# Optimization experiments

Measured on AMD Instinct MI355X. Metric: run time of the kernel, lower is better.

The kernel has to match this reference:

```python
import jax, jax.numpy as jnp
import numpy as np

CHEB_K = 3
HIDDEN = 64
INPUT_DIM = 2
B, N = 16, 307


def setup_inputs() -> dict:
    key = jax.random.key(0)
    ks = jax.random.split(key, 7)
    in_dim = CHEB_K * (INPUT_DIM + HIDDEN)  # 198
    return {
        "G": jax.random.normal(ks[0], (CHEB_K, N, N), jnp.float32) / np.sqrt(N),
        "xt": jax.random.normal(ks[1], (B, N, INPUT_DIM), jnp.float32),
        "h": jax.random.normal(ks[2], (B, N, HIDDEN), jnp.float32),
        "W_conv_gate": jax.random.normal(ks[3], (B, N, in_dim, 2 * HIDDEN), jnp.float32) * 0.05,
        "b_conv_gate": jax.random.normal(ks[4], (B, N, 2 * HIDDEN), jnp.float32) * 0.05,
        "W_update": jax.random.normal(ks[5], (B, N, in_dim, HIDDEN), jnp.float32) * 0.05,
        "b_update": jax.random.normal(ks[6], (B, N, HIDDEN), jnp.float32) * 0.05,
    }


def _st_meta_gcn(G, x, W, b):
    # G: [K,N,N], x: [B,N,I] -> support per hop, concatenated hop-major on feat axis
    bsz, n, i = x.shape
    sup = jnp.einsum('knm,bmi->bnki', G, x)          # [B,N,K,I]
    sup = sup.reshape(bsz, n, G.shape[0] * i)        # matches torch.cat over hops
    return jnp.einsum('bni,bnih->bnh', sup, W) + b


def reference(G, xt, h, W_conv_gate, b_conv_gate, W_update, b_update):
    combined = jnp.concatenate([xt, h], axis=-1)
    gates = jax.nn.sigmoid(_st_meta_gcn(G, combined, W_conv_gate, b_conv_gate))
    z, r = gates[..., :HIDDEN], gates[..., HIDDEN:]
    candidate = jnp.concatenate([xt, r * h], axis=-1)
    n = jnp.tanh(_st_meta_gcn(G, candidate, W_update, b_update))
    return z * n + (1.0 - z) * h
```

## Files before the change

kernel.cpp:

```cpp
#include <hip/hip_runtime.h>
#include <math.h>

#define NB   16
#define NN   307
#define MPAD 308
#define Q4   77
#define KCH  3
#define IND  66
#define KI   198
#define HID  64
#define HG   128

typedef float f32x4 __attribute__((ext_vector_type(4)));

#define OFF_GP  0
#define SZ_GP   (KCH * NN * MPAD)
#define OFF_X1  (OFF_GP + SZ_GP)
#define SZ_X    (NB * Q4 * IND * 4)
#define OFF_X2  (OFF_X1 + SZ_X)
#define OFF_Z   (OFF_X2 + SZ_X)

__global__ void prep_kernel(const float* __restrict__ G,
                            const float* __restrict__ xt,
                            const float* __restrict__ h,
                            float* __restrict__ G_p,
                            float* __restrict__ x1,
                            float* __restrict__ x2) {
    int idx = blockIdx.x * blockDim.x + threadIdx.x;
    if (idx < SZ_GP) {
        int mp = idx % MPAD;
        int kn = idx / MPAD;
        G_p[idx] = (mp < NN) ? G[kn * NN + mp] : 0.f;
    } else if (idx < SZ_GP + SZ_X) {
        int j = idx - SZ_GP;
        int e = j & 3;
        int t = j >> 2;
        int i = t % IND;
        int q = (t / IND) % Q4;
        int b = t / (IND * Q4);
        int m = q * 4 + e;
        float v = 0.f;
        if (m < NN)
            v = (i < 2) ? xt[(b * NN + m) * 2 + i]
                        : h[(b * NN + m) * HID + (i - 2)];
        x1[j] = v;
    } else if (idx < SZ_GP + 2 * SZ_X) {
        int j = idx - SZ_GP - SZ_X;
        int e = j & 3;
        int t = j >> 2;
        int i = t % IND;
        int q = (t / IND) % Q4;
        int b = t / (IND * Q4);
        int m = q * 4 + e;
        float v = 0.f;
        if (m < NN && i < 2) v = xt[(b * NN + m) * 2 + i];
        x2[j] = v;
    }
}

__global__ __launch_bounds__(128) void gate_fused(const float* __restrict__ G_p,
                                                  const float* __restrict__ xT,
                                                  const float* __restrict__ W,
                                                  const float* __restrict__ bias,
                                                  const float* __restrict__ h,
                                                  float* __restrict__ z_out,
                                                  float* __restrict__ xT2) {
    __shared__ float s[KI];
    __shared__ float red[4][HG];
    const int bn  = blockIdx.x;
    const int b   = bn / NN;
    const int n   = bn % NN;
    const int tid = threadIdx.x;
    if (tid < IND) {
        const f32x4* xp = (const f32x4*)xT + (size_t)b * (Q4 * IND) + tid;
        const f32x4* gp = (const f32x4*)G_p + (size_t)n * Q4;
        f32x4 a0 = {0.f, 0.f, 0.f, 0.f}, a1 = a0, a2 = a0;
        #pragma unroll 7
        for (int q = 0; q < Q4; ++q) {
            f32x4 xv = xp[(size_t)q * IND];
            a0 += xv * gp[q];
            a1 += xv * gp[q + (size_t)NN * Q4];
            a2 += xv * gp[q + (size_t)2 * NN * Q4];
        }
        s[tid]           = a0.x + a0.y + a0.z + a0.w;
        s[IND + tid]     = a1.x + a1.y + a1.z + a1.w;
        s[2 * IND + tid] = a2.x + a2.y + a2.z + a2.w;
    }
    __syncthreads();
    const int r  = tid >> 5;
    const int c4 = (tid & 31) * 4;
    const f32x4* Wp = (const f32x4*)(W + (size_t)bn * KI * HG + c4);
    float4 acc = make_float4(0.f, 0.f, 0.f, 0.f);
    #pragma unroll 8
    for (int i = r; i < KI; i += 4) {
        f32x4 w = __builtin_nontemporal_load(Wp + (size_t)i * (HG / 4));
        float sv = s[i];
        acc.x += sv * w.x; acc.y += sv * w.y;
        acc.z += sv * w.z; acc.w += sv * w.w;
    }
    red[r][c4 + 0] = acc.x; red[r][c4 + 1] = acc.y;
    red[r][c4 + 2] = acc.z; red[r][c4 + 3] = acc.w;
    __syncthreads();
    float a = bias[bn * HG + tid] + red[0][tid] + red[1][tid] + red[2][tid] + red[3][tid];
    float g = 1.0f / (1.0f + expf(-a));
    if (tid < HID) {
        z_out[bn * HID + tid] = g;
    } else {
        int hh = tid - HID;
        int q = n >> 2, e = n & 3;
        xT2[(((size_t)b * Q4 + q) * IND + 2 + hh) * 4 + e] = g * h[bn * HID + hh];
    }
}

__global__ __launch_bounds__(128) void update_fused(const float* __restrict__ G_p,
                                                    const float* __restrict__ xT2,
                                                    const float* __restrict__ W,
                                                    const float* __restrict__ bias,
                                                    const float* __restrict__ z,
                                                    const float* __restrict__ h,
                                                    float* __restrict__ out) {
    __shared__ float s[KI];
    __shared__ float red[8][HID];
    const int bn  = blockIdx.x;
    const int b   = bn / NN;
    const int n   = bn % NN;
    const int tid = threadIdx.x;
    if (tid < IND) {
        const f32x4* xp = (const f32x4*)xT2 + (size_t)b * (Q4 * IND) + tid;
        const f32x4* gp = (const f32x4*)G_p + (size_t)n * Q4;
        f32x4 a0 = {0.f, 0.f, 0.f, 0.f}, a1 = a0, a2 = a0;
        #pragma unroll 7
        for (int q = 0; q < Q4; ++q) {
            f32x4 xv = xp[(size_t)q * IND];
            a0 += xv * gp[q];
            a1 += xv * gp[q + (size_t)NN * Q4];
            a2 += xv * gp[q + (size_t)2 * NN * Q4];
        }
        s[tid]           = a0.x + a0.y + a0.z + a0.w;
        s[IND + tid]     = a1.x + a1.y + a1.z + a1.w;
        s[2 * IND + tid] = a2.x + a2.y + a2.z + a2.w;
    }
    __syncthreads();
    const int r  = tid >> 4;
    const int c4 = (tid & 15) * 4;
    const f32x4* Wp = (const f32x4*)(W + (size_t)bn * KI * HID + c4);
    float4 acc = make_float4(0.f, 0.f, 0.f, 0.f);
    #pragma unroll 8
    for (int i = r; i < KI; i += 8) {
        f32x4 w = __builtin_nontemporal_load(Wp + (size_t)i * (HID / 4));
        float sv = s[i];
        acc.x += sv * w.x; acc.y += sv * w.y;
        acc.z += sv * w.z; acc.w += sv * w.w;
    }
    red[r][c4 + 0] = acc.x; red[r][c4 + 1] = acc.y;
    red[r][c4 + 2] = acc.z; red[r][c4 + 3] = acc.w;
    __syncthreads();
    if (tid < HID) {
        float a = bias[bn * HID + tid];
        #pragma unroll
        for (int rr = 0; rr < 8; ++rr) a += red[rr][tid];
        float nn = tanhf(a);
        float zz = z[bn * HID + tid];
        float hv = h[bn * HID + tid];
        out[bn * HID + tid] = zz * nn + (1.f - zz) * hv;
    }
}

extern "C" void kernel_launch(void* const* d_in, const int* in_sizes, int n_in,
                              void* d_out, int out_size, void* d_ws, size_t ws_size,
                              hipStream_t stream) {
    const float* G  = (const float*)d_in[0];
    const float* xt = (const float*)d_in[1];
    const float* h  = (const float*)d_in[2];
    const float* Wg = (const float*)d_in[3];
    const float* bg = (const float*)d_in[4];
    const float* Wu = (const float*)d_in[5];
    const float* bu = (const float*)d_in[6];
    float* out = (float*)d_out;

    float* ws   = (float*)d_ws;
    float* G_p  = ws + OFF_GP;
    float* x1   = ws + OFF_X1;
    float* x2   = ws + OFF_X2;
    float* z    = ws + OFF_Z;

    const int totPrep = SZ_GP + 2 * SZ_X;
    prep_kernel<<<(totPrep + 255) / 256, 256, 0, stream>>>(G, xt, h, G_p, x1, x2);

    gate_fused<<<NB * NN, 128, 0, stream>>>(G_p, x1, Wg, bg, h, z, x2);

    update_fused<<<NB * NN, 128, 0, stream>>>(G_p, x2, Wu, bu, z, h, out);
}
```

Measured before the change: 164.0 us.

## Prefetch per-node weights during graph aggregation and shrink x2 prep to input channels

Each block now issues its first ten weight-row loads into registers, spread across the graph-support loop, so the streaming of W overlaps the G·x aggregation rather than starting after the barrier. All threads run the aggregation loop (clamped index) so every thread can interleave its prefetches, and only the first 66 threads store results. The prep kernel no longer zero-fills all of x2; it writes only the two xt channels, because the gate kernel overwrites the rest. This costs more registers per thread and redundant aggregation work in idle threads.

```diff
diff --git a/kernel.cpp b/kernel.cpp
--- a/kernel.cpp
+++ b/kernel.cpp
@@ -19,6 +19,7 @@
 #define SZ_X    (NB * Q4 * IND * 4)
 #define OFF_X2  (OFF_X1 + SZ_X)
 #define OFF_Z   (OFF_X2 + SZ_X)
+#define SZ_X2I  (NB * Q4 * 2 * 4)
 
 __global__ void prep_kernel(const float* __restrict__ G,
                             const float* __restrict__ xt,
@@ -44,17 +45,17 @@
             v = (i < 2) ? xt[(b * NN + m) * 2 + i]
                         : h[(b * NN + m) * HID + (i - 2)];
         x1[j] = v;
-    } else if (idx < SZ_GP + 2 * SZ_X) {
+    } else if (idx < SZ_GP + SZ_X + SZ_X2I) {
         int j = idx - SZ_GP - SZ_X;
-        int e = j & 3;
-        int t = j >> 2;
-        int i = t % IND;
-        int q = (t / IND) % Q4;
-        int b = t / (IND * Q4);
-        int m = q * 4 + e;
-        float v = 0.f;
-        if (m < NN && i < 2) v = xt[(b * NN + m) * 2 + i];
-        x2[j] = v;
+        int e  = j & 3;
+        int t  = j >> 2;
+        int i  = t & 1;
+        int t2 = t >> 1;
+        int q  = t2 % Q4;
+        int b  = t2 / Q4;
+        int m  = q * 4 + e;
+        float v = (m < NN) ? xt[(b * NN + m) * 2 + i] : 0.f;
+        x2[(((size_t)b * Q4 + q) * IND + i) * 4 + e] = v;
     }
 }
 
@@ -71,33 +72,51 @@
     const int b   = bn / NN;
     const int n   = bn % NN;
     const int tid = threadIdx.x;
+    const int r   = tid >> 5;
+    const int c4  = (tid & 31) * 4;
+    const f32x4* Wp = (const f32x4*)(W + (size_t)bn * KI * HG + c4);
+    const int ii = (tid < IND) ? tid : 0;
+    const f32x4* xp = (const f32x4*)xT + (size_t)b * (Q4 * IND) + ii;
+    const f32x4* gp = (const f32x4*)G_p + (size_t)n * Q4;
+    f32x4 a0 = {0.f, 0.f, 0.f, 0.f}, a1 = a0, a2 = a0;
+    f32x4 w0, w1, w2, w3, w4, w5, w6, w7, w8, w9;
+    #pragma unroll
+    for (int q = 0; q < Q4; ++q) {
+        if (q == 0)  w0 = __builtin_nontemporal_load(Wp + (size_t)(r +  0) * (HG / 4));
+        if (q == 8)  w1 = __builtin_nontemporal_load(Wp + (size_t)(r +  4) * (HG / 4));
+        if (q == 16) w2 = __builtin_nontemporal_load(Wp + (size_t)(r +  8) * (HG / 4));
+        if (q == 24) w3 = __builtin_nontemporal_load(Wp + (size_t)(r + 12) * (HG / 4));
+        if (q == 32) w4 = __builtin_nontemporal_load(Wp + (size_t)(r + 16) * (HG / 4));
+        if (q == 40) w5 = __builtin_nontemporal_load(Wp + (size_t)(r + 20) * (HG / 4));
+        if (q == 48) w6 = __builtin_nontemporal_load(Wp + (size_t)(r + 24) * (HG / 4));
+        if (q == 56) w7 = __builtin_nontemporal_load(Wp + (size_t)(r + 28) * (HG / 4));
+        if (q == 64) w8 = __builtin_nontemporal_load(Wp + (size_t)(r + 32) * (HG / 4));
+        if (q == 72) w9 = __builtin_nontemporal_load(Wp + (size_t)(r + 36) * (HG / 4));
+        f32x4 xv = xp[(size_t)q * IND];
+        a0 += xv * gp[q];
+        a1 += xv * gp[q + (size_t)NN * Q4];
+        a2 += xv * gp[q + (size_t)2 * NN * Q4];
+    }
     if (tid < IND) {
-        const f32x4* xp = (const f32x4*)xT + (size_t)b * (Q4 * IND) + tid;
-        const f32x4* gp = (const f32x4*)G_p + (size_t)n * Q4;
-        f32x4 a0 = {0.f, 0.f, 0.f, 0.f}, a1 = a0, a2 = a0;
-        #pragma unroll 7
-        for (int q = 0; q < Q4; ++q) {
-            f32x4 xv = xp[(size_t)q * IND];
-            a0 += xv * gp[q];
-            a1 += xv * gp[q + (size_t)NN * Q4];
-            a2 += xv * gp[q + (size_t)2 * NN * Q4];
-        }
         s[tid]           = a0.x + a0.y + a0.z + a0.w;
         s[IND + tid]     = a1.x + a1.y + a1.z + a1.w;
         s[2 * IND + tid] = a2.x + a2.y + a2.z + a2.w;
     }
     __syncthreads();
-    const int r  = tid >> 5;
-    const int c4 = (tid & 31) * 4;
-    const f32x4* Wp = (const f32x4*)(W + (size_t)bn * KI * HG + c4);
     float4 acc = make_float4(0.f, 0.f, 0.f, 0.f);
+#define CONS(wv, I) { float sv = s[(I)]; acc.x += sv * (wv).x; acc.y += sv * (wv).y; \
+                      acc.z += sv * (wv).z; acc.w += sv * (wv).w; }
+    CONS(w0, r)      CONS(w1, r + 4)  CONS(w2, r + 8)  CONS(w3, r + 12)
+    CONS(w4, r + 16) CONS(w5, r + 20) CONS(w6, r + 24) CONS(w7, r + 28)
+    CONS(w8, r + 32) CONS(w9, r + 36)
     #pragma unroll 8
-    for (int i = r; i < KI; i += 4) {
+    for (int i = r + 40; i < KI; i += 4) {
         f32x4 w = __builtin_nontemporal_load(Wp + (size_t)i * (HG / 4));
         float sv = s[i];
         acc.x += sv * w.x; acc.y += sv * w.y;
         acc.z += sv * w.z; acc.w += sv * w.w;
     }
+#undef CONS
     red[r][c4 + 0] = acc.x; red[r][c4 + 1] = acc.y;
     red[r][c4 + 2] = acc.z; red[r][c4 + 3] = acc.w;
     __syncthreads();
@@ -125,33 +144,51 @@
     const int b   = bn / NN;
     const int n   = bn % NN;
     const int tid = threadIdx.x;
+    const int r   = tid >> 4;
+    const int c4  = (tid & 15) * 4;
+    const f32x4* Wp = (const f32x4*)(W + (size_t)bn * KI * HID + c4);
+    const int ii = (tid < IND) ? tid : 0;
+    const f32x4* xp = (const f32x4*)xT2 + (size_t)b * (Q4 * IND) + ii;
+    const f32x4* gp = (const f32x4*)G_p + (size_t)n * Q4;
+    f32x4 a0 = {0.f, 0.f, 0.f, 0.f}, a1 = a0, a2 = a0;
+    f32x4 w0, w1, w2, w3, w4, w5, w6, w7, w8, w9;
+    #pragma unroll
+    for (int q = 0; q < Q4; ++q) {
+        if (q == 0)  w0 = __builtin_nontemporal_load(Wp + (size_t)(r +  0) * (HID / 4));
+        if (q == 8)  w1 = __builtin_nontemporal_load(Wp + (size_t)(r +  8) * (HID / 4));
+        if (q == 16) w2 = __builtin_nontemporal_load(Wp + (size_t)(r + 16) * (HID / 4));
+        if (q == 24) w3 = __builtin_nontemporal_load(Wp + (size_t)(r + 24) * (HID / 4));
+        if (q == 32) w4 = __builtin_nontemporal_load(Wp + (size_t)(r + 32) * (HID / 4));
+        if (q == 40) w5 = __builtin_nontemporal_load(Wp + (size_t)(r + 40) * (HID / 4));
+        if (q == 48) w6 = __builtin_nontemporal_load(Wp + (size_t)(r + 48) * (HID / 4));
+        if (q == 56) w7 = __builtin_nontemporal_load(Wp + (size_t)(r + 56) * (HID / 4));
+        if (q == 64) w8 = __builtin_nontemporal_load(Wp + (size_t)(r + 64) * (HID / 4));
+        if (q == 72) w9 = __builtin_nontemporal_load(Wp + (size_t)(r + 72) * (HID / 4));
+        f32x4 xv = xp[(size_t)q * IND];
+        a0 += xv * gp[q];
+        a1 += xv * gp[q + (size_t)NN * Q4];
+        a2 += xv * gp[q + (size_t)2 * NN * Q4];
+    }
     if (tid < IND) {
-        const f32x4* xp = (const f32x4*)xT2 + (size_t)b * (Q4 * IND) + tid;
-        const f32x4* gp = (const f32x4*)G_p + (size_t)n * Q4;
-        f32x4 a0 = {0.f, 0.f, 0.f, 0.f}, a1 = a0, a2 = a0;
-        #pragma unroll 7
-        for (int q = 0; q < Q4; ++q) {
-            f32x4 xv = xp[(size_t)q * IND];
-            a0 += xv * gp[q];
-            a1 += xv * gp[q + (size_t)NN * Q4];
-            a2 += xv * gp[q + (size_t)2 * NN * Q4];
-        }
         s[tid]           = a0.x + a0.y + a0.z + a0.w;
         s[IND + tid]     = a1.x + a1.y + a1.z + a1.w;
         s[2 * IND + tid] = a2.x + a2.y + a2.z + a2.w;
     }
     __syncthreads();
-    const int r  = tid >> 4;
-    const int c4 = (tid & 15) * 4;
-    const f32x4* Wp = (const f32x4*)(W + (size_t)bn * KI * HID + c4);
     float4 acc = make_float4(0.f, 0.f, 0.f, 0.f);
+#define CONS(wv, I) { float sv = s[(I)]; acc.x += sv * (wv).x; acc.y += sv * (wv).y; \
+                      acc.z += sv * (wv).z; acc.w += sv * (wv).w; }
+    CONS(w0, r)      CONS(w1, r + 8)  CONS(w2, r + 16) CONS(w3, r + 24)
+    CONS(w4, r + 32) CONS(w5, r + 40) CONS(w6, r + 48) CONS(w7, r + 56)
+    CONS(w8, r + 64) CONS(w9, r + 72)
     #pragma unroll 8
-    for (int i = r; i < KI; i += 8) {
+    for (int i = r + 80; i < KI; i += 8) {
         f32x4 w = __builtin_nontemporal_load(Wp + (size_t)i * (HID / 4));
         float sv = s[i];
         acc.x += sv * w.x; acc.y += sv * w.y;
         acc.z += sv * w.z; acc.w += sv * w.w;
     }
+#undef CONS
     red[r][c4 + 0] = acc.x; red[r][c4 + 1] = acc.y;
     red[r][c4 + 2] = acc.z; red[r][c4 + 3] = acc.w;
     __syncthreads();
@@ -184,7 +221,7 @@
     float* x2   = ws + OFF_X2;
     float* z    = ws + OFF_Z;
 
-    const int totPrep = SZ_GP + 2 * SZ_X;
+    const int totPrep = SZ_GP + SZ_X + SZ_X2I;
     prep_kernel<<<(totPrep + 255) / 256, 256, 0, stream>>>(G, xt, h, G_p, x1, x2);
 
     gate_fused<<<NB * NN, 128, 0, stream>>>(G_p, x1, Wg, bg, h, z, x2);
```

Measured after the change: 172.1 us. 5.0% more time.

## Process four nodes per block with per-wave phase1 sharing x loads

Applied to the files above, without the earlier changes.

Each 128-thread block now handles four nodes (two per wave) instead of one. The graph-support phase reuses each x load across two nodes and uses all 64 lanes, with the two leftover features computed via a shuffle reduction. The W matvec now uses all lanes, reduces with cross-lane shuffles instead of shared-memory reduction and barriers, and writes vectorized outputs. The prep kernel only writes the xt columns of x2 rather than the whole buffer. The aim is less idle-lane time, fewer barriers and less redundant traffic, at the cost of fewer, heavier blocks and more registers per thread.

```diff
diff --git a/kernel.cpp b/kernel.cpp
--- a/kernel.cpp
+++ b/kernel.cpp
@@ -3,13 +3,14 @@
 
 #define NB   16
 #define NN   307
+#define Q4   77
 #define MPAD 308
-#define Q4   77
 #define KCH  3
 #define IND  66
 #define KI   198
 #define HID  64
 #define HG   128
+#define NG   77
 
 typedef float f32x4 __attribute__((ext_vector_type(4)));
 
@@ -19,6 +20,7 @@
 #define SZ_X    (NB * Q4 * IND * 4)
 #define OFF_X2  (OFF_X1 + SZ_X)
 #define OFF_Z   (OFF_X2 + SZ_X)
+#define SZ_X2I  (NB * Q4 * 2 * 4)
 
 __global__ void prep_kernel(const float* __restrict__ G,
                             const float* __restrict__ xt,
@@ -44,17 +46,75 @@
             v = (i < 2) ? xt[(b * NN + m) * 2 + i]
                         : h[(b * NN + m) * HID + (i - 2)];
         x1[j] = v;
-    } else if (idx < SZ_GP + 2 * SZ_X) {
+    } else if (idx < SZ_GP + SZ_X + SZ_X2I) {
         int j = idx - SZ_GP - SZ_X;
-        int e = j & 3;
-        int t = j >> 2;
-        int i = t % IND;
-        int q = (t / IND) % Q4;
-        int b = t / (IND * Q4);
-        int m = q * 4 + e;
-        float v = 0.f;
-        if (m < NN && i < 2) v = xt[(b * NN + m) * 2 + i];
-        x2[j] = v;
+        int e  = j & 3;
+        int t  = j >> 2;
+        int i  = t & 1;
+        int t2 = t >> 1;
+        int q  = t2 % Q4;
+        int b  = t2 / Q4;
+        int m  = q * 4 + e;
+        float v = (m < NN) ? xt[(b * NN + m) * 2 + i] : 0.f;
+        x2[(((size_t)b * Q4 + q) * IND + i) * 4 + e] = v;
+    }
+}
+
+__device__ __forceinline__ void phase1_wave(const f32x4* __restrict__ G4,
+                                            const f32x4* __restrict__ X4,
+                                            int b, int na, int nb,
+                                            float* __restrict__ sA,
+                                            float* __restrict__ sB,
+                                            int lane) {
+    const int nac = (na < NN) ? na : (NN - 1);
+    const int nbc = (nb < NN) ? nb : (NN - 1);
+    const f32x4* xp  = X4 + (size_t)b * (Q4 * IND) + lane;
+    const f32x4* gA0 = G4 + ((size_t)0 * NN + nac) * Q4;
+    const f32x4* gA1 = G4 + ((size_t)1 * NN + nac) * Q4;
+    const f32x4* gA2 = G4 + ((size_t)2 * NN + nac) * Q4;
+    const f32x4* gB0 = G4 + ((size_t)0 * NN + nbc) * Q4;
+    const f32x4* gB1 = G4 + ((size_t)1 * NN + nbc) * Q4;
+    const f32x4* gB2 = G4 + ((size_t)2 * NN + nbc) * Q4;
+    f32x4 aA0 = {0.f,0.f,0.f,0.f}, aA1 = aA0, aA2 = aA0;
+    f32x4 aB0 = aA0, aB1 = aA0, aB2 = aA0;
+    #pragma unroll 7
+    for (int q = 0; q < Q4; ++q) {
+        f32x4 xv = xp[(size_t)q * IND];
+        aA0 += xv * gA0[q];  aA1 += xv * gA1[q];  aA2 += xv * gA2[q];
+        aB0 += xv * gB0[q];  aB1 += xv * gB1[q];  aB2 += xv * gB2[q];
+    }
+    sA[0 * IND + lane] = aA0.x + aA0.y + aA0.z + aA0.w;
+    sA[1 * IND + lane] = aA1.x + aA1.y + aA1.z + aA1.w;
+    sA[2 * IND + lane] = aA2.x + aA2.y + aA2.z + aA2.w;
+    sB[0 * IND + lane] = aB0.x + aB0.y + aB0.z + aB0.w;
+    sB[1 * IND + lane] = aB1.x + aB1.y + aB1.z + aB1.w;
+    sB[2 * IND + lane] = aB2.x + aB2.y + aB2.z + aB2.w;
+    const int j  = lane >> 4;
+    const int sl = lane & 15;
+    const int ns = j >> 1;
+    const int it = 64 + (j & 1);
+    const int nt = ns ? nbc : nac;
+    f32x4 t0 = {0.f,0.f,0.f,0.f}, t1 = t0, t2 = t0;
+    for (int q = sl; q < Q4; q += 16) {
+        f32x4 xv = X4[(size_t)b * (Q4 * IND) + (size_t)q * IND + it];
+        t0 += xv * G4[((size_t)0 * NN + nt) * Q4 + q];
+        t1 += xv * G4[((size_t)1 * NN + nt) * Q4 + q];
+        t2 += xv * G4[((size_t)2 * NN + nt) * Q4 + q];
+    }
+    float h0 = t0.x + t0.y + t0.z + t0.w;
+    float h1 = t1.x + t1.y + t1.z + t1.w;
+    float h2 = t2.x + t2.y + t2.z + t2.w;
+    #pragma unroll
+    for (int m = 1; m < 16; m <<= 1) {
+        h0 += __shfl_xor(h0, m);
+        h1 += __shfl_xor(h1, m);
+        h2 += __shfl_xor(h2, m);
+    }
+    if (sl == 0) {
+        float* sp = ns ? sB : sA;
+        sp[0 * IND + it] = h0;
+        sp[1 * IND + it] = h1;
+        sp[2 * IND + it] = h2;
     }
 }
 
@@ -65,50 +125,54 @@
                                                   const float* __restrict__ h,
                                                   float* __restrict__ z_out,
                                                   float* __restrict__ xT2) {
-    __shared__ float s[KI];
-    __shared__ float red[4][HG];
-    const int bn  = blockIdx.x;
-    const int b   = bn / NN;
-    const int n   = bn % NN;
-    const int tid = threadIdx.x;
-    if (tid < IND) {
-        const f32x4* xp = (const f32x4*)xT + (size_t)b * (Q4 * IND) + tid;
-        const f32x4* gp = (const f32x4*)G_p + (size_t)n * Q4;
-        f32x4 a0 = {0.f, 0.f, 0.f, 0.f}, a1 = a0, a2 = a0;
-        #pragma unroll 7
-        for (int q = 0; q < Q4; ++q) {
-            f32x4 xv = xp[(size_t)q * IND];
-            a0 += xv * gp[q];
-            a1 += xv * gp[q + (size_t)NN * Q4];
-            a2 += xv * gp[q + (size_t)2 * NN * Q4];
-        }
-        s[tid]           = a0.x + a0.y + a0.z + a0.w;
-        s[IND + tid]     = a1.x + a1.y + a1.z + a1.w;
-        s[2 * IND + tid] = a2.x + a2.y + a2.z + a2.w;
-    }
-    __syncthreads();
-    const int r  = tid >> 5;
-    const int c4 = (tid & 31) * 4;
-    const f32x4* Wp = (const f32x4*)(W + (size_t)bn * KI * HG + c4);
-    float4 acc = make_float4(0.f, 0.f, 0.f, 0.f);
-    #pragma unroll 8
-    for (int i = r; i < KI; i += 4) {
-        f32x4 w = __builtin_nontemporal_load(Wp + (size_t)i * (HG / 4));
-        float sv = s[i];
-        acc.x += sv * w.x; acc.y += sv * w.y;
-        acc.z += sv * w.z; acc.w += sv * w.w;
-    }
-    red[r][c4 + 0] = acc.x; red[r][c4 + 1] = acc.y;
-    red[r][c4 + 2] = acc.z; red[r][c4 + 3] = acc.w;
-    __syncthreads();
-    float a = bias[bn * HG + tid] + red[0][tid] + red[1][tid] + red[2][tid] + red[3][tid];
-    float g = 1.0f / (1.0f + expf(-a));
-    if (tid < HID) {
-        z_out[bn * HID + tid] = g;
-    } else {
-        int hh = tid - HID;
-        int q = n >> 2, e = n & 3;
-        xT2[(((size_t)b * Q4 + q) * IND + 2 + hh) * 4 + e] = g * h[bn * HID + hh];
+    __shared__ float s[4][KI];
+    const int blk  = blockIdx.x;
+    const int b    = blk / NG;
+    const int n0   = (blk % NG) * 4;
+    const int wave = threadIdx.x >> 6;
+    const int lane = threadIdx.x & 63;
+    const int na   = n0 + wave * 2;
+    const int nb   = na + 1;
+    phase1_wave((const f32x4*)G_p, (const f32x4*)xT, b, na, nb,
+                s[wave * 2], s[wave * 2 + 1], lane);
+    const int c = lane & 31;
+    const int r = lane >> 5;
+    #pragma unroll
+    for (int ps = 0; ps < 2; ++ps) {
+        const int n   = na + ps;
+        const int bnc = b * NN + ((n < NN) ? n : (NN - 1));
+        const f32x4* Wp = (const f32x4*)W + (size_t)bnc * KI * (HG / 4) + c;
+        const float* sp = s[wave * 2 + ps];
+        f32x4 acc = {0.f,0.f,0.f,0.f};
+        #pragma unroll 16
+        for (int i = r; i < KI; i += 2) {
+            f32x4 w = __builtin_nontemporal_load(Wp + (size_t)i * (HG / 4));
+            acc += w * sp[i];
+        }
+        acc.x += __shfl_xor(acc.x, 32);
+        acc.y += __shfl_xor(acc.y, 32);
+        acc.z += __shfl_xor(acc.z, 32);
+        acc.w += __shfl_xor(acc.w, 32);
+        if (lane < 32 && n < NN) {
+            const int bn = b * NN + n;
+            f32x4 bv = ((const f32x4*)bias)[(size_t)bn * (HG / 4) + c];
+            f32x4 a  = acc + bv;
+            float g0 = 1.0f / (1.0f + expf(-a.x));
+            float g1 = 1.0f / (1.0f + expf(-a.y));
+            float g2 = 1.0f / (1.0f + expf(-a.z));
+            float g3 = 1.0f / (1.0f + expf(-a.w));
+            if (c < 16) {
+                f32x4 zv = {g0, g1, g2, g3};
+                ((f32x4*)z_out)[(size_t)bn * (HID / 4) + c] = zv;
+            } else {
+                int hh0 = (c - 16) * 4;
+                size_t base = (((size_t)b * Q4 + (n >> 2)) * IND) * 4 + (n & 3);
+                xT2[base + (size_t)(2 + hh0 + 0) * 4] = g0 * h[bn * HID + hh0 + 0];
+                xT2[base + (size_t)(2 + hh0 + 1) * 4] = g1 * h[bn * HID + hh0 + 1];
+                xT2[base + (size_t)(2 + hh0 + 2) * 4] = g2 * h[bn * HID + hh0 + 2];
+                xT2[base + (size_t)(2 + hh0 + 3) * 4] = g3 * h[bn * HID + hh0 + 3];
+            }
+        }
     }
 }
 
@@ -119,50 +183,51 @@
                                                     const float* __restrict__ z,
                                                     const float* __restrict__ h,
                                                     float* __restrict__ out) {
-    __shared__ float s[KI];
-    __shared__ float red[8][HID];
-    const int bn  = blockIdx.x;
-    const int b   = bn / NN;
-    const int n   = bn % NN;
-    const int tid = threadIdx.x;
-    if (tid < IND) {
-        const f32x4* xp = (const f32x4*)xT2 + (size_t)b * (Q4 * IND) + tid;
-        const f32x4* gp = (const f32x4*)G_p + (size_t)n * Q4;
-        f32x4 a0 = {0.f, 0.f, 0.f, 0.f}, a1 = a0, a2 = a0;
-        #pragma unroll 7
-        for (int q = 0; q < Q4; ++q) {
-            f32x4 xv = xp[(size_t)q * IND];
-            a0 += xv * gp[q];
-            a1 += xv * gp[q + (size_t)NN * Q4];
-            a2 += xv * gp[q + (size_t)2 * NN * Q4];
-        }
-        s[tid]           = a0.x + a0.y + a0.z + a0.w;
-        s[IND + tid]     = a1.x + a1.y + a1.z + a1.w;
-        s[2 * IND + tid] = a2.x + a2.y + a2.z + a2.w;
-    }
-    __syncthreads();
-    const int r  = tid >> 4;
-    const int c4 = (tid & 15) * 4;
-    const f32x4* Wp = (const f32x4*)(W + (size_t)bn * KI * HID + c4);
-    float4 acc = make_float4(0.f, 0.f, 0.f, 0.f);
-    #pragma unroll 8
-    for (int i = r; i < KI; i += 8) {
-        f32x4 w = __builtin_nontemporal_load(Wp + (size_t)i * (HID / 4));
-        float sv = s[i];
-        acc.x += sv * w.x; acc.y += sv * w.y;
-        acc.z += sv * w.z; acc.w += sv * w.w;
-    }
-    red[r][c4 + 0] = acc.x; red[r][c4 + 1] = acc.y;
-    red[r][c4 + 2] = acc.z; red[r][c4 + 3] = acc.w;
-    __syncthreads();
-    if (tid < HID) {
-        float a = bias[bn * HID + tid];
-        #pragma unroll
-        for (int rr = 0; rr < 8; ++rr) a += red[rr][tid];
-        float nn = tanhf(a);
-        float zz = z[bn * HID + tid];
-        float hv = h[bn * HID + tid];
-        out[bn * HID + tid] = zz * nn + (1.f - zz) * hv;
+    __shared__ float s[4][KI];
+    const int blk  = blockIdx.x;
+    const int b    = blk / NG;
+    const int n0   = (blk % NG) * 4;
+    const int wave = threadIdx.x >> 6;
+    const int lane = threadIdx.x & 63;
+    const int na   = n0 + wave * 2;
+    const int nb   = na + 1;
+    phase1_wave((const f32x4*)G_p, (const f32x4*)xT2, b, na, nb,
+                s[wave * 2], s[wave * 2 + 1], lane);
+    const int c = lane & 15;
+    const int r = lane >> 4;
+    #pragma unroll
+    for (int ps = 0; ps < 2; ++ps) {
+        const int n   = na + ps;
+        const int bnc = b * NN + ((n < NN) ? n : (NN - 1));
+        const f32x4* Wp = (const f32x4*)W + (size_t)bnc * KI * (HID / 4) + c;
+        const float* sp = s[wave * 2 + ps];
+        f32x4 acc = {0.f,0.f,0.f,0.f};
+        #pragma unroll 16
+        for (int i = r; i < KI; i += 4) {
+            f32x4 w = __builtin_nontemporal_load(Wp + (size_t)i * (HID / 4));
+            acc += w * sp[i];
+        }
+        acc.x += __shfl_xor(acc.x, 16);
+        acc.y += __shfl_xor(acc.y, 16);
+        acc.z += __shfl_xor(acc.z, 16);
+        acc.w += __shfl_xor(acc.w, 16);
+        acc.x += __shfl_xor(acc.x, 32);
+        acc.y += __shfl_xor(acc.y, 32);
+        acc.z += __shfl_xor(acc.z, 32);
+        acc.w += __shfl_xor(acc.w, 32);
+        if (lane < 16 && n < NN) {
+            const int bn = b * NN + n;
+            f32x4 bv = ((const f32x4*)bias)[(size_t)bn * (HID / 4) + c];
+            f32x4 a  = acc + bv;
+            f32x4 zz = ((const f32x4*)z)[(size_t)bn * (HID / 4) + c];
+            f32x4 hv = ((const f32x4*)h)[(size_t)bn * (HID / 4) + c];
+            f32x4 o;
+            o.x = zz.x * tanhf(a.x) + (1.f - zz.x) * hv.x;
+            o.y = zz.y * tanhf(a.y) + (1.f - zz.y) * hv.y;
+            o.z = zz.z * tanhf(a.z) + (1.f - zz.z) * hv.z;
+            o.w = zz.w * tanhf(a.w) + (1.f - zz.w) * hv.w;
+            ((f32x4*)out)[(size_t)bn * (HID / 4) + c] = o;
+        }
     }
 }
 
@@ -184,10 +249,10 @@
     float* x2   = ws + OFF_X2;
     float* z    = ws + OFF_Z;
 
-    const int totPrep = SZ_GP + 2 * SZ_X;
+    const int totPrep = SZ_GP + SZ_X + SZ_X2I;
     prep_kernel<<<(totPrep + 255) / 256, 256, 0, stream>>>(G, xt, h, G_p, x1, x2);
 
-    gate_fused<<<NB * NN, 128, 0, stream>>>(G_p, x1, Wg, bg, h, z, x2);
-
-    update_fused<<<NB * NN, 128, 0, stream>>>(G_p, x2, Wu, bu, z, h, out);
-}
+    gate_fused<<<NB * NG, 128, 0, stream>>>(G_p, x1, Wg, bg, h, z, x2);
+
+    update_fused<<<NB * NG, 128, 0, stream>>>(G_p, x2, Wu, bu, z, h, out);
+}
```

Result: slower. 222.8 us (+35.8%).

## Split graph-support phase across both waves and shrink x2 prep to xt columns

Applied to the files above, without the earlier changes.

The G·x support computation, previously done by only 66 threads in one wave, is now split across both 64-lane waves by interleaving the q range. The two leftover feature columns are handled by wave 0 with a shuffle reduction, and the partial sums are combined through shared memory. The prep kernel now writes only the two xt columns of x2, since gate_fused overwrites the h part anyway. This trades an extra shared-memory reduction and barrier for better use of the block's threads and less prep work.

```diff
diff --git a/kernel.cpp b/kernel.cpp
--- a/kernel.cpp
+++ b/kernel.cpp
@@ -19,6 +19,7 @@
 #define SZ_X    (NB * Q4 * IND * 4)
 #define OFF_X2  (OFF_X1 + SZ_X)
 #define OFF_Z   (OFF_X2 + SZ_X)
+#define SZ_X2I  (NB * Q4 * 2 * 4)
 
 __global__ void prep_kernel(const float* __restrict__ G,
                             const float* __restrict__ xt,
@@ -44,18 +45,75 @@
             v = (i < 2) ? xt[(b * NN + m) * 2 + i]
                         : h[(b * NN + m) * HID + (i - 2)];
         x1[j] = v;
-    } else if (idx < SZ_GP + 2 * SZ_X) {
+    } else if (idx < SZ_GP + SZ_X + SZ_X2I) {
         int j = idx - SZ_GP - SZ_X;
-        int e = j & 3;
-        int t = j >> 2;
-        int i = t % IND;
-        int q = (t / IND) % Q4;
-        int b = t / (IND * Q4);
-        int m = q * 4 + e;
-        float v = 0.f;
-        if (m < NN && i < 2) v = xt[(b * NN + m) * 2 + i];
-        x2[j] = v;
-    }
+        int e  = j & 3;
+        int t  = j >> 2;
+        int i  = t & 1;
+        int t2 = t >> 1;
+        int q  = t2 % Q4;
+        int b  = t2 / Q4;
+        int m  = q * 4 + e;
+        float v = (m < NN) ? xt[(b * NN + m) * 2 + i] : 0.f;
+        x2[(((size_t)b * Q4 + q) * IND + i) * 4 + e] = v;
+    }
+}
+
+__device__ __forceinline__ void phase1_block(const f32x4* __restrict__ G4,
+                                             const f32x4* __restrict__ X4,
+                                             int b, int n, int tid,
+                                             float part[2][KCH][IND],
+                                             float* __restrict__ s) {
+    const int wave = tid >> 6;
+    const int lane = tid & 63;
+    const f32x4* xp = X4 + (size_t)b * (Q4 * IND) + lane;
+    const f32x4* g0 = G4 + ((size_t)0 * NN + n) * Q4;
+    const f32x4* g1 = G4 + ((size_t)1 * NN + n) * Q4;
+    const f32x4* g2 = G4 + ((size_t)2 * NN + n) * Q4;
+    f32x4 a0 = {0.f,0.f,0.f,0.f}, a1 = a0, a2 = a0;
+    #pragma unroll 8
+    for (int q = wave; q < Q4; q += 2) {
+        f32x4 xv = xp[(size_t)q * IND];
+        a0 += xv * g0[q];
+        a1 += xv * g1[q];
+        a2 += xv * g2[q];
+    }
+    part[wave][0][lane] = a0.x + a0.y + a0.z + a0.w;
+    part[wave][1][lane] = a1.x + a1.y + a1.z + a1.w;
+    part[wave][2][lane] = a2.x + a2.y + a2.z + a2.w;
+    if (wave == 0) {
+        const int it = 64 + (lane >> 5);
+        const int sl = lane & 31;
+        f32x4 t0 = {0.f,0.f,0.f,0.f}, t1 = t0, t2 = t0;
+        for (int q = sl; q < Q4; q += 32) {
+            f32x4 xv = X4[(size_t)b * (Q4 * IND) + (size_t)q * IND + it];
+            t0 += xv * g0[q];
+            t1 += xv * g1[q];
+            t2 += xv * g2[q];
+        }
+        float h0 = t0.x + t0.y + t0.z + t0.w;
+        float h1 = t1.x + t1.y + t1.z + t1.w;
+        float h2 = t2.x + t2.y + t2.z + t2.w;
+        #pragma unroll
+        for (int m = 1; m < 32; m <<= 1) {
+            h0 += __shfl_xor(h0, m);
+            h1 += __shfl_xor(h1, m);
+            h2 += __shfl_xor(h2, m);
+        }
+        if (sl == 0) {
+            part[0][0][it] = h0;
+            part[0][1][it] = h1;
+            part[0][2][it] = h2;
+        }
+    } else if (lane < 6) {
+        part[1][lane >> 1][64 + (lane & 1)] = 0.f;
+    }
+    __syncthreads();
+    for (int t = tid; t < KI; t += 128) {
+        int k = t / IND, i = t % IND;
+        s[t] = part[0][k][i] + part[1][k][i];
+    }
+    __syncthreads();
 }
 
 __global__ __launch_bounds__(128) void gate_fused(const float* __restrict__ G_p,
@@ -65,28 +123,14 @@
                                                   const float* __restrict__ h,
                                                   float* __restrict__ z_out,
                                                   float* __restrict__ xT2) {
+    __shared__ float part[2][KCH][IND];
     __shared__ float s[KI];
     __shared__ float red[4][HG];
     const int bn  = blockIdx.x;
     const int b   = bn / NN;
     const int n   = bn % NN;
     const int tid = threadIdx.x;
-    if (tid < IND) {
-        const f32x4* xp = (const f32x4*)xT + (size_t)b * (Q4 * IND) + tid;
-        const f32x4* gp = (const f32x4*)G_p + (size_t)n * Q4;
-        f32x4 a0 = {0.f, 0.f, 0.f, 0.f}, a1 = a0, a2 = a0;
-        #pragma unroll 7
-        for (int q = 0; q < Q4; ++q) {
-            f32x4 xv = xp[(size_t)q * IND];
-            a0 += xv * gp[q];
-            a1 += xv * gp[q + (size_t)NN * Q4];
-            a2 += xv * gp[q + (size_t)2 * NN * Q4];
-        }
-        s[tid]           = a0.x + a0.y + a0.z + a0.w;
-        s[IND + tid]     = a1.x + a1.y + a1.z + a1.w;
-        s[2 * IND + tid] = a2.x + a2.y + a2.z + a2.w;
-    }
-    __syncthreads();
+    phase1_block((const f32x4*)G_p, (const f32x4*)xT, b, n, tid, part, s);
     const int r  = tid >> 5;
     const int c4 = (tid & 31) * 4;
     const f32x4* Wp = (const f32x4*)(W + (size_t)bn * KI * HG + c4);
@@ -119,28 +163,14 @@
                                                     const float* __restrict__ z,
                                                     const float* __restrict__ h,
                                                     float* __restrict__ out) {
+    __shared__ float part[2][KCH][IND];
     __shared__ float s[KI];
     __shared__ float red[8][HID];
     const int bn  = blockIdx.x;
     const int b   = bn / NN;
     const int n   = bn % NN;
     const int tid = threadIdx.x;
-    if (tid < IND) {
-        const f32x4* xp = (const f32x4*)xT2 + (size_t)b * (Q4 * IND) + tid;
-        const f32x4* gp = (const f32x4*)G_p + (size_t)n * Q4;
-        f32x4 a0 = {0.f, 0.f, 0.f, 0.f}, a1 = a0, a2 = a0;
-        #pragma unroll 7
-        for (int q = 0; q < Q4; ++q) {
-            f32x4 xv = xp[(size_t)q * IND];
-            a0 += xv * gp[q];
-            a1 += xv * gp[q + (size_t)NN * Q4];
-            a2 += xv * gp[q + (size_t)2 * NN * Q4];
-        }
-        s[tid]           = a0.x + a0.y + a0.z + a0.w;
-        s[IND + tid]     = a1.x + a1.y + a1.z + a1.w;
-        s[2 * IND + tid] = a2.x + a2.y + a2.z + a2.w;
-    }
-    __syncthreads();
+    phase1_block((const f32x4*)G_p, (const f32x4*)xT2, b, n, tid, part, s);
     const int r  = tid >> 4;
     const int c4 = (tid & 15) * 4;
     const f32x4* Wp = (const f32x4*)(W + (size_t)bn * KI * HID + c4);
@@ -184,7 +214,7 @@
     float* x2   = ws + OFF_X2;
     float* z    = ws + OFF_Z;
 
-    const int totPrep = SZ_GP + 2 * SZ_X;
+    const int totPrep = SZ_GP + SZ_X + SZ_X2I;
     prep_kernel<<<(totPrep + 255) / 256, 256, 0, stream>>>(G, xt, h, G_p, x1, x2);
 
     gate_fused<<<NB * NN, 128, 0, stream>>>(G_p, x1, Wg, bg, h, z, x2);
```

Result: slower. 211.3 us (+28.8%).
